# Kernel optimization log

Measured on AMD Instinct MI355X. Metric: run time of the kernel, lower is better.

The kernel has to match this reference:

```python
import jax, jax.numpy as jnp
import numpy as np
import math

V, L, D, S, F, H, B = 32000, 6, 1024, 2048, 4096, 16, 2
DK = D // H
EPS = 1e-5


def _pos_encoding(max_len, d_model):
    pos = np.arange(max_len)[:, None].astype(np.float32)
    freq = np.exp(np.arange(0, d_model, 2).astype(np.float32) * -(math.log(10000.0) / d_model))
    pe = np.zeros((max_len, d_model), dtype=np.float32)
    pe[:, 0::2] = np.sin(pos * freq)
    pe[:, 1::2] = np.cos(pos * freq)
    return jnp.asarray(pe)


def setup_inputs() -> dict:
    key = jax.random.key(0)
    ks = jax.random.split(key, 16)
    n = lambda k, shape: (jax.random.normal(k, shape, dtype=jnp.float32) * 0.02)
    return {
        "tokens": jax.random.randint(ks[0], (B, S), 0, V, dtype=jnp.int32),
        "emb": n(ks[1], (V, D)),
        "Wq": n(ks[2], (L, D, D)), "bq": jnp.zeros((L, D)),
        "Wk": n(ks[3], (L, D, D)), "bk": jnp.zeros((L, D)),
        "Wv": n(ks[4], (L, D, D)), "bv": jnp.zeros((L, D)),
        "Wo": n(ks[5], (L, D, D)), "bo": jnp.zeros((L, D)),
        "W1": n(ks[6], (L, D, F)), "b1": jnp.zeros((L, F)),
        "W2": n(ks[7], (L, F, D)), "b2": jnp.zeros((L, D)),
        "g1": jnp.ones((L, D)), "be1": jnp.zeros((L, D)),
        "g2": jnp.ones((L, D)), "be2": jnp.zeros((L, D)),
    }


def _layernorm(x, g, b):
    mu = jnp.mean(x, axis=-1, keepdims=True)
    var = jnp.var(x, axis=-1, keepdims=True)
    return (x - mu) * jax.lax.rsqrt(var + EPS) * g + b


def _encoder(tokens, emb, Wq, bq, Wk, bk, Wv, bv, Wo, bo, W1, b1, W2, b2, g1, be1, g2, be2):
    pe = _pos_encoding(S, D)
    x = emb[tokens] * jnp.float32(math.sqrt(D)) + pe  # [B,S,D]

    def layer(x, p):
        wq, bq_, wk, bk_, wv, bv_, wo, bo_, w1, b1_, w2, b2_, g1_, be1_, g2_, be2_ = p
        q = (x @ wq + bq_).reshape(B, S, H, DK)
        k = (x @ wk + bk_).reshape(B, S, H, DK)
        v = (x @ wv + bv_).reshape(B, S, H, DK)
        scores = jnp.einsum("bqhd,bkhd->bhqk", q, k) / jnp.float32(math.sqrt(DK))
        attn = jax.nn.softmax(scores, axis=-1)
        out = jnp.einsum("bhqk,bkhd->bqhd", attn, v).reshape(B, S, D)
        out = out @ wo + bo_
        x = _layernorm(x + out, g1_, be1_)
        ff = jax.nn.relu(x @ w1 + b1_) @ w2 + b2_
        x = _layernorm(x + ff, g2_, be2_)
        return x, None

    params = (Wq, bq, Wk, bk, Wv, bv, Wo, bo, W1, b1, W2, b2, g1, be1, g2, be2)
    x, _ = jax.lax.scan(layer, x, params)
    return x


def reference(tokens, emb, Wq, bq, Wk, bk, Wv, bv, Wo, bo, W1, b1, W2, b2, g1, be1, g2, be2):
    return _encoder(tokens, emb, Wq, bq, Wk, bk, Wv, bv, Wo, bo, W1, b1, W2, b2, g1, be1, g2, be2)
```

## Files before the change

kernel.cpp:

```cpp
#include <hip/hip_runtime.h>
#include <hip/hip_bf16.h>

#define DEV static __device__ __forceinline__

typedef __attribute__((ext_vector_type(8))) short bf16x8;
typedef __attribute__((ext_vector_type(4))) float f32x4;
typedef __attribute__((ext_vector_type(4))) unsigned short u16x4;
typedef __attribute__((ext_vector_type(4))) unsigned int u32x4;

constexpr int Lc = 6, Dc = 1024, Sc = 2048, Fc = 4096, Hc = 16, Bc = 2;
constexpr int Mc = Bc * Sc;
constexpr int QKVN = 3 * Dc;
constexpr float QSCALE = 0.18033688011112042f;

DEV float bf2f(unsigned short u) {
  unsigned int x = ((unsigned int)u) << 16; float f;
  __builtin_memcpy(&f, &x, 4); return f;
}
DEV unsigned short f2bf(float f) {
  unsigned int x; __builtin_memcpy(&x, &f, 4);
  x += 0x7fffu + ((x >> 16) & 1u);
  return (unsigned short)(x >> 16);
}
DEV unsigned int cvt_pk_bf16(float lo, float hi) {
  unsigned int r;
  asm("v_cvt_pk_bf16_f32 %0, %1, %2" : "=v"(r) : "v"(lo), "v"(hi));
  return r;
}

typedef __attribute__((address_space(1))) unsigned int* gas_t;
typedef __attribute__((address_space(3))) unsigned int* las_t;
DEV void gload16(const void* g, void* l) {
  __builtin_amdgcn_global_load_lds((gas_t)g, (las_t)l, 16, 0, 0);
}

DEV int vperm(int k) {
  return ((k >> 5) << 5) + (((k >> 2) & 3) << 3) + (((k >> 4) & 1) << 2) + (k & 3);
}

DEV void tr64(const float* __restrict__ W, unsigned short* __restrict__ Wt,
              int Kd, int Nd, float scale, int bx, int by, int tid,
              float (*tile)[33])
{
  const int n0 = bx * 32;
  const int tx = tid & 31, krow = tid >> 5;
  const int w = tid >> 6, lane = tid & 63;
#pragma unroll
  for (int s = 0; s < 4; ++s) {
    const int k0 = by * 256 + s * 64;
#pragma unroll
    for (int j = 0; j < 8; ++j) {
      int k = krow + j * 8;
      tile[k][tx] = W[(size_t)(k0 + k) * Nd + n0 + tx];
    }
    __syncthreads();
#pragma unroll
    for (int j = 0; j < 8; ++j) {
      int n = w * 8 + j;
      Wt[(size_t)(n0 + n) * Kd + k0 + lane] = f2bf(tile[lane][n] * scale);
    }
    __syncthreads();
  }
}

__global__ __launch_bounds__(256) void prep_weights(
    const float* __restrict__ Wq, const float* __restrict__ Wk,
    const float* __restrict__ Wv, const float* __restrict__ Wo,
    const float* __restrict__ W1, const float* __restrict__ W2,
    const float* __restrict__ bq, const float* __restrict__ bk,
    const float* __restrict__ bv,
    unsigned short* __restrict__ Wqkvt, unsigned short* __restrict__ Wot,
    unsigned short* __restrict__ W1t, unsigned short* __restrict__ W2t,
    float* __restrict__ bqkv)
{
  __shared__ float tile[64][33];
  const int l = blockIdx.x / 1548;
  const int id = blockIdx.x % 1548;
  const int t = threadIdx.x;
  const size_t owD = (size_t)l * Dc * Dc, owF = (size_t)l * Dc * Fc;
  unsigned short* Wqkvt_l = Wqkvt + (size_t)l * 3 * Dc * Dc;
  unsigned short* Wot_l = Wot + (size_t)l * Dc * Dc;
  unsigned short* W1t_l = W1t + owF;
  unsigned short* W2t_l = W2t + owF;
  if (id < 512) {
    int which = id >> 7, lo = id & 127;
    int bx = lo & 31, by = lo >> 5;
    if (which == 0)      tr64(Wq + owD, Wqkvt_l, Dc, Dc, QSCALE, bx, by, t, tile);
    else if (which == 1) tr64(Wk + owD, Wqkvt_l + (size_t)Dc * Dc, Dc, Dc, 1.0f, bx, by, t, tile);
    else if (which == 2) tr64(Wv + owD, Wqkvt_l + (size_t)2 * Dc * Dc, Dc, Dc, 1.0f, bx, by, t, tile);
    else                 tr64(Wo + owD, Wot_l, Dc, Dc, 1.0f, bx, by, t, tile);
  } else if (id < 1024) {
    int lo = id - 512;
    tr64(W1 + owF, W1t_l, Dc, Fc, 1.0f, lo & 127, lo >> 7, t, tile);
  } else if (id < 1536) {
    int lo = id - 1024;
    tr64(W2 + owF, W2t_l, Fc, Dc, 1.0f, lo & 31, lo >> 5, t, tile);
  } else {
    int i = (id - 1536) * 256 + t;
    const int ob = l * Dc;
    bqkv[l * QKVN + i] =
        (i < Dc) ? bq[ob + i] * QSCALE
                 : (i < 2 * Dc ? bk[ob + i - Dc] : bv[ob + i - 2 * Dc]);
  }
}

__global__ __launch_bounds__(256) void embed_kernel(
    const int* __restrict__ tokens, const float* __restrict__ emb,
    float* __restrict__ xf, unsigned short* __restrict__ xb)
{
  const int bs = blockIdx.x;
  const int s = bs & (Sc - 1);
  const int tok = tokens[bs];
  const int d0 = threadIdx.x * 4;
  f32x4 e4 = *(const f32x4*)(emb + (size_t)tok * Dc + d0);
  f32x4 vf; u16x4 vb;
#pragma unroll
  for (int j = 0; j < 4; ++j) {
    int d = d0 + j;
    float e = e4[j] * 32.0f;
    float fr = expf((float)(d & ~1) * (-9.210340371976184f / 1024.0f));
    float arg = (float)s * fr;
    float pe = (d & 1) ? cosf(arg) : sinf(arg);
    float v = e + pe;
    vf[j] = v; vb[j] = f2bf(v);
  }
  *(f32x4*)(xf + (size_t)bs * Dc + d0) = vf;
  *(u16x4*)(xb + (size_t)bs * Dc + d0) = vb;
}

DEV void gemm256_core(const unsigned short* __restrict__ A,
                      const unsigned short* __restrict__ Bt,
                      unsigned short (*As)[256 * 64], unsigned short (*Bs)[256 * 64],
                      f32x4 (*acc)[4], int mTile, int nTile,
                      int Kstride, int k0, int nT, int t)
{
  const int lane = t & 63;
  const int g = lane >> 4, li = lane & 15;
  const int w = t >> 6;
  const int wm = w >> 2, wn = w & 3;
  const int trow = t >> 3, tslot = t & 7;
  const int asl = tslot ^ (trow & 7);
  int aoff[4];
#pragma unroll
  for (int q = 0; q < 4; ++q) {
    int R = (trow < 32) ? (q * 32 + trow) : (96 + q * 32 + trow);
    aoff[q] = (mTile + R) * Kstride + k0 + asl * 8;
  }
  int boff[4], bld[4];
#pragma unroll
  for (int k2 = 0; k2 < 4; ++k2) {
    int idx = k2 * 512 + t;
    int br = idx >> 3;
    int bs = (idx & 7) ^ (br & 7);
    boff[k2] = (nTile + br) * Kstride + k0 + bs * 8;
    bld[k2] = idx * 8;
  }

  auto stB = [&](int nb, int kt, int ph) {
    gload16(Bt + boff[ph * 2 + 0] + kt, &Bs[nb][bld[ph * 2 + 0]]);
    gload16(Bt + boff[ph * 2 + 1] + kt, &Bs[nb][bld[ph * 2 + 1]]);
  };
  auto stA = [&](int nb, int kt, int ph) {
    gload16(A + aoff[ph * 2 + 0] + kt, &As[nb][(ph * 2 + 0) * 4096 + t * 8]);
    gload16(A + aoff[ph * 2 + 1] + kt, &As[nb][(ph * 2 + 1) * 4096 + t * 8]);
  };

  stB(0, 0, 0); stB(0, 0, 1); stA(0, 0, 0); stA(0, 0, 1);
  asm volatile("s_waitcnt vmcnt(0)" ::: "memory");
  __builtin_amdgcn_s_barrier();

  int cur = 0;
  for (int tt = 0; tt < nT; ++tt) {
    const char* Ac = (const char*)As[cur];
    const char* Bc = (const char*)Bs[cur];
    const int nb = cur ^ 1;
    const int ktn = (tt + 1) << 6;
    const bool more = tt + 1 < nT;

    bf16x8 bfr[4][2];
#pragma unroll
    for (int ni = 0; ni < 4; ++ni) {
      const int rn = wn * 64 + ni * 16 + li;
#pragma unroll
      for (int ks = 0; ks < 2; ++ks) {
        const int kb = ks * 64 + (g << 4);
        bfr[ni][ks] = *(const bf16x8*)(Bc + rn * 128 + (kb ^ ((rn & 7) << 4)));
      }
    }

#pragma unroll
    for (int ph = 0; ph < 4; ++ph) {
      bf16x8 afr[2][2];
#pragma unroll
      for (int mi2 = 0; mi2 < 2; ++mi2) {
        const int rr = wm * 32 + mi2 * 16 + li;
#pragma unroll
        for (int ks = 0; ks < 2; ++ks) {
          const int kb = ks * 64 + (g << 4);
          afr[mi2][ks] = *(const bf16x8*)(Ac + ph * 8192 + rr * 128 + (kb ^ ((rr & 7) << 4)));
        }
      }
      if (more) {
        if (ph == 0)      stB(nb, ktn, 0);
        else if (ph == 1) stB(nb, ktn, 1);
        else if (ph == 2) stA(nb, ktn, 0);
        else              stA(nb, ktn, 1);
      }
      __builtin_amdgcn_s_barrier();
      __builtin_amdgcn_s_setprio(1);
#pragma unroll
      for (int mi2 = 0; mi2 < 2; ++mi2)
#pragma unroll
        for (int ni = 0; ni < 4; ++ni)
#pragma unroll
          for (int ks = 0; ks < 2; ++ks)
            acc[ph * 2 + mi2][ni] = __builtin_amdgcn_mfma_f32_16x16x32_bf16(
                afr[mi2][ks], bfr[ni][ks], acc[ph * 2 + mi2][ni], 0, 0, 0);
      __builtin_amdgcn_s_setprio(0);
      if (ph == 0)      asm volatile("s_waitcnt vmcnt(4)" ::: "memory");
      else if (ph == 1) asm volatile("s_waitcnt vmcnt(5)" ::: "memory");
      else if (ph == 2) asm volatile("s_waitcnt vmcnt(6)" ::: "memory");
      else              asm volatile("s_waitcnt vmcnt(3)" ::: "memory");
      __builtin_amdgcn_s_barrier();
    }
    cur ^= 1;
  }
}

__global__ __launch_bounds__(512) void gemm256(
    const unsigned short* __restrict__ A, const unsigned short* __restrict__ Bt,
    const float* __restrict__ bias, unsigned short* __restrict__ outB,
    unsigned short* __restrict__ Vt, int gx, int Ndim, int Kdim, int relu)
{
  __shared__ alignas(16) unsigned short As[2][256 * 64];
  __shared__ alignas(16) unsigned short Bs[2][256 * 64];
  const int t = threadIdx.x;
  const int lane = t & 63, w = t >> 6;
  const int wm = w >> 2, wn = w & 3;
  const int g = lane >> 4, li = lane & 15;
  const int nwg = gridDim.x, flat = blockIdx.x;
  const int swz = (flat & 7) * (nwg >> 3) + (flat >> 3);
  const int mTile = (swz / gx) * 256;
  const int nTile = (swz % gx) * 256;

  f32x4 acc[8][4] = {};
  gemm256_core(A, Bt, As, Bs, acc, mTile, nTile, Kdim, 0, Kdim >> 6, t);

  const bool vblk = (Vt != nullptr) && (nTile >= 2 * Dc);
#pragma unroll
  for (int mi = 0; mi < 8; ++mi) {
#pragma unroll
    for (int ni = 0; ni < 4; ++ni) {
      const int c = nTile + wn * 64 + ni * 16 + li;
      const float bvv = bias[c];
      if (!vblk) {
#pragma unroll
        for (int j = 0; j < 4; ++j) {
          const int r = mTile + wm * 128 + mi * 16 + g * 4 + j;
          float v = acc[mi][ni][j] + bvv;
          if (relu) v = fmaxf(v, 0.0f);
          outB[(size_t)r * Ndim + c] = f2bf(v);
        }
      } else {
        const int r0 = mTile + wm * 128 + mi * 16 + g * 4;
        const int b = r0 >> 11, s0 = r0 & 2047;
        const int sp = (s0 & ~63) + vperm(s0 & 63);
        u16x4 ov;
#pragma unroll
        for (int j = 0; j < 4; ++j) ov[j] = f2bf(acc[mi][ni][j] + bvv);
        *(u16x4*)(Vt + ((size_t)(b * Dc + (c - 2 * Dc))) * Sc + sp) = ov;
      }
    }
  }
}

template<int SPLIT>
__global__ __launch_bounds__(512) void gemm256_sk(
    const unsigned short* __restrict__ A, const unsigned short* __restrict__ Bt,
    unsigned short* __restrict__ part, int gx, int gy, int Ndim, int Ktot)
{
  __shared__ alignas(16) unsigned short As[2][256 * 64];
  __shared__ alignas(16) unsigned short Bs[2][256 * 64];
  const int t = threadIdx.x;
  const int lane = t & 63, w = t >> 6;
  const int wm = w >> 2, wn = w & 3;
  const int g = lane >> 4, li = lane & 15;
  const int nwg = gridDim.x, flat = blockIdx.x;
  const int swz = (flat & 7) * (nwg >> 3) + (flat >> 3);
  const int nTile = (swz % gx) * 256;
  const int mTile = ((swz / gx) % gy) * 256;
  const int z = swz / (gx * gy);
  const int Kseg = Ktot / SPLIT;

  f32x4 acc[8][4] = {};
  gemm256_core(A, Bt, As, Bs, acc, mTile, nTile, Ktot, z * Kseg, Kseg >> 6, t);

  unsigned short* po = part + (size_t)z * Mc * Ndim;
#pragma unroll
  for (int mi = 0; mi < 8; ++mi)
#pragma unroll
    for (int ni = 0; ni < 4; ++ni) {
      const int c = nTile + wn * 64 + ni * 16 + li;
#pragma unroll
      for (int j = 0; j < 4; ++j) {
        const int r = mTile + wm * 128 + mi * 16 + g * 4 + j;
        po[(size_t)r * Ndim + c] = f2bf(acc[mi][ni][j]);
      }
    }
}

__global__ __launch_bounds__(256) void attn128(
    const unsigned short* __restrict__ QKV, const unsigned short* __restrict__ Vt,
    unsigned short* __restrict__ O)
{
  __shared__ alignas(16) unsigned short Qs[128 * 64];
  __shared__ alignas(16) unsigned short Ks[2][64 * 64];
  __shared__ alignas(16) unsigned short Vs[2][64 * 64];

  const int t = threadIdx.x;
  const int lane = t & 63, w = t >> 6;
  const int g = lane >> 4, li = lane & 15;
  const int flat = blockIdx.x;
  const int idx = ((flat & 7) << 6) | (flat >> 3);
  const int qb = idx & 15, bh = idx >> 4;
  const int b = bh >> 4, h = bh & 15;

  const size_t qbase  = ((size_t)(b * Sc + qb * 128)) * QKVN + h * 64;
  const size_t kbase0 = ((size_t)b * Sc) * QKVN + Dc + h * 64;
  const size_t vbase0 = ((size_t)(b * Dc + h * 64)) * Sc;

#pragma unroll
  for (int i = 0; i < 4; ++i) {
    int idx2 = i * 256 + t, row = idx2 >> 3, sl = (idx2 & 7) ^ (row & 7);
    gload16(QKV + qbase + (size_t)row * QKVN + sl * 8, &Qs[idx2 * 8]);
  }
  const unsigned short* kg[2];
  const unsigned short* vg[2];
  int loff[2];
#pragma unroll
  for (int i = 0; i < 2; ++i) {
    int idx2 = i * 256 + t, row = idx2 >> 3, sl = (idx2 & 7) ^ (row & 7);
    kg[i] = QKV + kbase0 + (size_t)row * QKVN + sl * 8;
    vg[i] = Vt + vbase0 + (size_t)row * Sc + sl * 8;
    loff[i] = idx2 * 8;
  }
  gload16(kg[0], &Ks[0][loff[0]]); gload16(kg[1], &Ks[0][loff[1]]);
  gload16(vg[0], &Vs[0][loff[0]]); gload16(vg[1], &Vs[0][loff[1]]);
  kg[0] += 64 * QKVN; kg[1] += 64 * QKVN;
  vg[0] += 64;        vg[1] += 64;
  __syncthreads();

  bf16x8 qf[2][2];
#pragma unroll
  for (int qi = 0; qi < 2; ++qi) {
    const int rq = w * 32 + qi * 16 + li;
#pragma unroll
    for (int ks = 0; ks < 2; ++ks) {
      const int kb = ks * 64 + (g << 4);
      qf[qi][ks] = *(const bf16x8*)((const char*)Qs + rq * 128 + (kb ^ ((rq & 7) << 4)));
    }
  }
  bf16x8 ones;
#pragma unroll
  for (int e = 0; e < 8; ++e) ones[e] = (short)0x3F80;

  f32x4 acc_o[2][4] = {};
  f32x4 acc_l[2] = {};
  int cur = 0;

  for (int kc = 0; kc < Sc; kc += 64) {
    if (kc + 64 < Sc) {
      const int nxt = cur ^ 1;
      gload16(kg[0], &Ks[nxt][loff[0]]); gload16(kg[1], &Ks[nxt][loff[1]]);
      gload16(vg[0], &Vs[nxt][loff[0]]); gload16(vg[1], &Vs[nxt][loff[1]]);
      kg[0] += 64 * QKVN; kg[1] += 64 * QKVN;
      vg[0] += 64;        vg[1] += 64;
    }

    f32x4 accs[2][4] = {};
#pragma unroll
    for (int ks = 0; ks < 2; ++ks) {
      const int kb = ks * 64 + (g << 4);
#pragma unroll
      for (int ni = 0; ni < 4; ++ni) {
        int rk = ni * 16 + li;
        bf16x8 ak = *(const bf16x8*)((const char*)Ks[cur] + rk * 128 + (kb ^ ((rk & 7) << 4)));
        accs[0][ni] = __builtin_amdgcn_mfma_f32_16x16x32_bf16(ak, qf[0][ks], accs[0][ni], 0, 0, 0);
        accs[1][ni] = __builtin_amdgcn_mfma_f32_16x16x32_bf16(ak, qf[1][ks], accs[1][ni], 0, 0, 0);
      }
    }

    unsigned int pk[2][4][2];
#pragma unroll
    for (int qi = 0; qi < 2; ++qi)
#pragma unroll
      for (int ni = 0; ni < 4; ++ni) {
        float p0 = exp2f(accs[qi][ni][0]);
        float p1 = exp2f(accs[qi][ni][1]);
        float p2 = exp2f(accs[qi][ni][2]);
        float p3 = exp2f(accs[qi][ni][3]);
        pk[qi][ni][0] = cvt_pk_bf16(p0, p1);
        pk[qi][ni][1] = cvt_pk_bf16(p2, p3);
      }

#pragma unroll
    for (int ks = 0; ks < 2; ++ks) {
      bf16x8 ap[2];
#pragma unroll
      for (int qi = 0; qi < 2; ++qi) {
        u32x4 av = {pk[qi][2 * ks][0], pk[qi][2 * ks][1],
                    pk[qi][2 * ks + 1][0], pk[qi][2 * ks + 1][1]};
        ap[qi] = __builtin_bit_cast(bf16x8, av);
        acc_l[qi] = __builtin_amdgcn_mfma_f32_16x16x32_bf16(ap[qi], ones, acc_l[qi], 0, 0, 0);
      }
      const int kb = ks * 64 + (g << 4);
#pragma unroll
      for (int ni = 0; ni < 4; ++ni) {
        int rd = ni * 16 + li;
        bf16x8 bv = *(const bf16x8*)((const char*)Vs[cur] + rd * 128 + (kb ^ ((rd & 7) << 4)));
        acc_o[0][ni] = __builtin_amdgcn_mfma_f32_16x16x32_bf16(ap[0], bv, acc_o[0][ni], 0, 0, 0);
        acc_o[1][ni] = __builtin_amdgcn_mfma_f32_16x16x32_bf16(ap[1], bv, acc_o[1][ni], 0, 0, 0);
      }
    }

    __syncthreads();
    cur ^= 1;
  }

  const size_t obase = ((size_t)(b * Sc + qb * 128)) * Dc + h * 64;
#pragma unroll
  for (int qi = 0; qi < 2; ++qi) {
    float denom[4];
#pragma unroll
    for (int j = 0; j < 4; ++j) denom[j] = 1.0f / acc_l[qi][j];
#pragma unroll
    for (int ni = 0; ni < 4; ++ni)
#pragma unroll
      for (int j = 0; j < 4; ++j) {
        int q = w * 32 + qi * 16 + g * 4 + j;
        O[obase + (size_t)q * Dc + ni * 16 + li] = f2bf(acc_o[qi][ni][j] * denom[j]);
      }
  }
}

template<int SPLIT>
__global__ __launch_bounds__(256) void reduce_ln(
    const unsigned short* __restrict__ part, const float* __restrict__ bias,
    const float* __restrict__ res, const float* __restrict__ g,
    const float* __restrict__ be, float* __restrict__ xf_out,
    unsigned short* __restrict__ xb_out)
{
  const int row = blockIdx.x, t = threadIdx.x;
  const size_t off = (size_t)row * Dc + t * 4;
  f32x4 v = *(const f32x4*)(res + off);
  v += *(const f32x4*)(bias + t * 4);
#pragma unroll
  for (int s = 0; s < SPLIT; ++s) {
    u16x4 pv = *(const u16x4*)(part + (size_t)s * Mc * Dc + off);
#pragma unroll
    for (int j = 0; j < 4; ++j) v[j] += bf2f(pv[j]);
  }

  float sm = v[0] + v[1] + v[2] + v[3];
  float q = v[0]*v[0] + v[1]*v[1] + v[2]*v[2] + v[3]*v[3];
#pragma unroll
  for (int o = 32; o; o >>= 1) {
    sm += __shfl_down(sm, o);
    q += __shfl_down(q, o);
  }
  __shared__ float rs_[4], rq_[4];
  const int lane = t & 63, w = t >> 6;
  if (lane == 0) { rs_[w] = sm; rq_[w] = q; }
  __syncthreads();
  sm = rs_[0] + rs_[1] + rs_[2] + rs_[3];
  q = rq_[0] + rq_[1] + rq_[2] + rq_[3];
  const float mu = sm * (1.0f / 1024.0f);
  const float var = q * (1.0f / 1024.0f) - mu * mu;
  const float rstd = rsqrtf(var + 1e-5f);
  f32x4 vg = *(const f32x4*)(g + t * 4);
  f32x4 vb = *(const f32x4*)(be + t * 4);
  f32x4 o; u16x4 ob;
#pragma unroll
  for (int j = 0; j < 4; ++j) {
    float val = (v[j] - mu) * rstd * vg[j] + vb[j];
    o[j] = val; ob[j] = f2bf(val);
  }
  *(f32x4*)(xf_out + off) = o;
  *(u16x4*)(xb_out + off) = ob;
}

extern "C" void kernel_launch(void* const* d_in, const int* in_sizes, int n_in,
                              void* d_out, int out_size, void* d_ws, size_t ws_size,
                              hipStream_t stream)
{
  (void)in_sizes; (void)n_in; (void)out_size; (void)ws_size;
  const int*   tokens = (const int*)d_in[0];
  const float* emb = (const float*)d_in[1];
  const float* Wq = (const float*)d_in[2];
  const float* bq = (const float*)d_in[3];
  const float* Wk = (const float*)d_in[4];
  const float* bk = (const float*)d_in[5];
  const float* Wv = (const float*)d_in[6];
  const float* bv = (const float*)d_in[7];
  const float* Wo = (const float*)d_in[8];
  const float* bo = (const float*)d_in[9];
  const float* W1 = (const float*)d_in[10];
  const float* b1 = (const float*)d_in[11];
  const float* W2 = (const float*)d_in[12];
  const float* b2 = (const float*)d_in[13];
  const float* g1 = (const float*)d_in[14];
  const float* be1 = (const float*)d_in[15];
  const float* g2 = (const float*)d_in[16];
  const float* be2 = (const float*)d_in[17];

  char* p = (char*)d_ws;
  auto take = [&](size_t bytes) { char* q = p; p += bytes; return q; };
  unsigned short* Wqkvt = (unsigned short*)take((size_t)Lc * 3 * Dc * Dc * 2);
  unsigned short* Wot = (unsigned short*)take((size_t)Lc * Dc * Dc * 2);
  unsigned short* W1t = (unsigned short*)take((size_t)Lc * Dc * Fc * 2);
  unsigned short* W2t = (unsigned short*)take((size_t)Lc * Fc * Dc * 2);
  float*          bqkv = (float*)take((size_t)Lc * QKVN * 4);
  float*          xf  = (float*)take((size_t)Mc * Dc * 4);
  unsigned short* xb  = (unsigned short*)take((size_t)Mc * Dc * 2);
  unsigned short* QKVb = (unsigned short*)take((size_t)Mc * QKVN * 2);
  unsigned short* Vtb = (unsigned short*)take((size_t)Bc * Dc * Sc * 2);
  unsigned short* Ob  = (unsigned short*)take((size_t)Mc * Dc * 2);
  unsigned short* ff1 = (unsigned short*)take((size_t)Mc * Fc * 2);
  unsigned short* part = QKVb;

  dim3 blk(256);
  prep_weights<<<dim3(Lc * 1548), blk, 0, stream>>>(
      Wq, Wk, Wv, Wo, W1, W2, bq, bk, bv, Wqkvt, Wot, W1t, W2t, bqkv);
  embed_kernel<<<dim3(Mc), blk, 0, stream>>>(tokens, emb, xf, xb);

  for (int l = 0; l < Lc; ++l) {
    const int ob = l * Dc;
    const unsigned short* Wqkvt_l = Wqkvt + (size_t)l * 3 * Dc * Dc;
    const unsigned short* Wot_l = Wot + (size_t)l * Dc * Dc;
    const unsigned short* W1t_l = W1t + (size_t)l * Dc * Fc;
    const unsigned short* W2t_l = W2t + (size_t)l * Fc * Dc;

    gemm256<<<dim3((Mc / 256) * (QKVN / 256)), dim3(512), 0, stream>>>(
        xb, Wqkvt_l, bqkv + l * QKVN, QKVb, Vtb, QKVN / 256, QKVN, Dc, 0);
    attn128<<<dim3(512), blk, 0, stream>>>(QKVb, Vtb, Ob);

    gemm256_sk<4><<<dim3((Dc / 256) * (Mc / 256) * 4), dim3(512), 0, stream>>>(
        Ob, Wot_l, part, Dc / 256, Mc / 256, Dc, Dc);
    reduce_ln<4><<<dim3(Mc), blk, 0, stream>>>(
        part, bo + ob, xf, g1 + ob, be1 + ob, xf, xb);

    gemm256<<<dim3((Mc / 256) * (Fc / 256)), dim3(512), 0, stream>>>(
        xb, W1t_l, b1 + l * Fc, ff1, nullptr, Fc / 256, Fc, Dc, 1);

    gemm256_sk<4><<<dim3((Dc / 256) * (Mc / 256) * 4), dim3(512), 0, stream>>>(
        ff1, W2t_l, part, Dc / 256, Mc / 256, Dc, Fc);
    reduce_ln<4><<<dim3(Mc), blk, 0, stream>>>(
        part, b2 + ob, xf, g2 + ob, be2 + ob,
        (l == Lc - 1) ? (float*)d_out : xf, xb);
  }
}
```

Measured before the change: 1.420 ms.

## Vectorize weight transpose tiles and drop fp32 residual stream for bf16

The weight-prep transpose now works on 64x64 tiles with 16-byte float4 loads and 8-byte packed bf16 stores, halving the block count. The fp32 residual buffer is also removed: the embedding writes only bf16, and each LayerNorm reads its residual from the bf16 activation and writes fp32 only for the final output. This cuts global memory traffic in prep_weights, embed and reduce_ln. In exchange the residual path is held only in bf16, which adds rounding error that accumulates across the layers.

```diff
diff --git a/kernel.cpp b/kernel.cpp
--- a/kernel.cpp
+++ b/kernel.cpp
@@ -38,26 +38,29 @@
   return ((k >> 5) << 5) + (((k >> 2) & 3) << 3) + (((k >> 4) & 1) << 2) + (k & 3);
 }
 
-DEV void tr64(const float* __restrict__ W, unsigned short* __restrict__ Wt,
-              int Kd, int Nd, float scale, int bx, int by, int tid,
-              float (*tile)[33])
-{
-  const int n0 = bx * 32;
-  const int tx = tid & 31, krow = tid >> 5;
-  const int w = tid >> 6, lane = tid & 63;
+DEV void tr64v(const float* __restrict__ W, unsigned short* __restrict__ Wt,
+               int Kd, int Nd, float scale, int bx, int by, int tid,
+               float (*tile)[65])
+{
+  const int n0 = bx * 64;
 #pragma unroll
   for (int s = 0; s < 4; ++s) {
     const int k0 = by * 256 + s * 64;
 #pragma unroll
-    for (int j = 0; j < 8; ++j) {
-      int k = krow + j * 8;
-      tile[k][tx] = W[(size_t)(k0 + k) * Nd + n0 + tx];
+    for (int it = 0; it < 4; ++it) {
+      int idx = it * 256 + tid;
+      int k = idx >> 4, c0 = (idx & 15) * 4;
+      *(f32x4*)&tile[k][c0] = *(const f32x4*)&W[(size_t)(k0 + k) * Nd + n0 + c0];
     }
     __syncthreads();
 #pragma unroll
-    for (int j = 0; j < 8; ++j) {
-      int n = w * 8 + j;
-      Wt[(size_t)(n0 + n) * Kd + k0 + lane] = f2bf(tile[lane][n] * scale);
+    for (int it = 0; it < 4; ++it) {
+      int idx = it * 256 + tid;
+      int n = idx >> 4, kc = (idx & 15) * 4;
+      u16x4 o;
+#pragma unroll
+      for (int j = 0; j < 4; ++j) o[j] = f2bf(tile[kc + j][n] * scale);
+      *(u16x4*)&Wt[(size_t)(n0 + n) * Kd + k0 + kc] = o;
     }
     __syncthreads();
   }
@@ -73,30 +76,30 @@
     unsigned short* __restrict__ W1t, unsigned short* __restrict__ W2t,
     float* __restrict__ bqkv)
 {
-  __shared__ float tile[64][33];
-  const int l = blockIdx.x / 1548;
-  const int id = blockIdx.x % 1548;
+  __shared__ float tile[64][65];
+  const int l = blockIdx.x / 780;
+  const int id = blockIdx.x % 780;
   const int t = threadIdx.x;
   const size_t owD = (size_t)l * Dc * Dc, owF = (size_t)l * Dc * Fc;
   unsigned short* Wqkvt_l = Wqkvt + (size_t)l * 3 * Dc * Dc;
   unsigned short* Wot_l = Wot + (size_t)l * Dc * Dc;
   unsigned short* W1t_l = W1t + owF;
   unsigned short* W2t_l = W2t + owF;
-  if (id < 512) {
-    int which = id >> 7, lo = id & 127;
-    int bx = lo & 31, by = lo >> 5;
-    if (which == 0)      tr64(Wq + owD, Wqkvt_l, Dc, Dc, QSCALE, bx, by, t, tile);
-    else if (which == 1) tr64(Wk + owD, Wqkvt_l + (size_t)Dc * Dc, Dc, Dc, 1.0f, bx, by, t, tile);
-    else if (which == 2) tr64(Wv + owD, Wqkvt_l + (size_t)2 * Dc * Dc, Dc, Dc, 1.0f, bx, by, t, tile);
-    else                 tr64(Wo + owD, Wot_l, Dc, Dc, 1.0f, bx, by, t, tile);
-  } else if (id < 1024) {
+  if (id < 256) {
+    int which = id >> 6, lo = id & 63;
+    int bx = lo & 15, by = lo >> 4;
+    if (which == 0)      tr64v(Wq + owD, Wqkvt_l, Dc, Dc, QSCALE, bx, by, t, tile);
+    else if (which == 1) tr64v(Wk + owD, Wqkvt_l + (size_t)Dc * Dc, Dc, Dc, 1.0f, bx, by, t, tile);
+    else if (which == 2) tr64v(Wv + owD, Wqkvt_l + (size_t)2 * Dc * Dc, Dc, Dc, 1.0f, bx, by, t, tile);
+    else                 tr64v(Wo + owD, Wot_l, Dc, Dc, 1.0f, bx, by, t, tile);
+  } else if (id < 512) {
+    int lo = id - 256;
+    tr64v(W1 + owF, W1t_l, Dc, Fc, 1.0f, lo & 63, lo >> 6, t, tile);
+  } else if (id < 768) {
     int lo = id - 512;
-    tr64(W1 + owF, W1t_l, Dc, Fc, 1.0f, lo & 127, lo >> 7, t, tile);
-  } else if (id < 1536) {
-    int lo = id - 1024;
-    tr64(W2 + owF, W2t_l, Fc, Dc, 1.0f, lo & 31, lo >> 5, t, tile);
+    tr64v(W2 + owF, W2t_l, Fc, Dc, 1.0f, lo & 15, lo >> 4, t, tile);
   } else {
-    int i = (id - 1536) * 256 + t;
+    int i = (id - 768) * 256 + t;
     const int ob = l * Dc;
     bqkv[l * QKVN + i] =
         (i < Dc) ? bq[ob + i] * QSCALE
@@ -106,14 +109,14 @@
 
 __global__ __launch_bounds__(256) void embed_kernel(
     const int* __restrict__ tokens, const float* __restrict__ emb,
-    float* __restrict__ xf, unsigned short* __restrict__ xb)
+    unsigned short* __restrict__ xb)
 {
   const int bs = blockIdx.x;
   const int s = bs & (Sc - 1);
   const int tok = tokens[bs];
   const int d0 = threadIdx.x * 4;
   f32x4 e4 = *(const f32x4*)(emb + (size_t)tok * Dc + d0);
-  f32x4 vf; u16x4 vb;
+  u16x4 vb;
 #pragma unroll
   for (int j = 0; j < 4; ++j) {
     int d = d0 + j;
@@ -121,10 +124,8 @@
     float fr = expf((float)(d & ~1) * (-9.210340371976184f / 1024.0f));
     float arg = (float)s * fr;
     float pe = (d & 1) ? cosf(arg) : sinf(arg);
-    float v = e + pe;
-    vf[j] = v; vb[j] = f2bf(v);
-  }
-  *(f32x4*)(xf + (size_t)bs * Dc + d0) = vf;
+    vb[j] = f2bf(e + pe);
+  }
   *(u16x4*)(xb + (size_t)bs * Dc + d0) = vb;
 }
 
@@ -446,13 +447,16 @@
 template<int SPLIT>
 __global__ __launch_bounds__(256) void reduce_ln(
     const unsigned short* __restrict__ part, const float* __restrict__ bias,
-    const float* __restrict__ res, const float* __restrict__ g,
-    const float* __restrict__ be, float* __restrict__ xf_out,
+    const unsigned short* __restrict__ resb, const float* __restrict__ g,
+    const float* __restrict__ be, float* __restrict__ fout,
     unsigned short* __restrict__ xb_out)
 {
   const int row = blockIdx.x, t = threadIdx.x;
   const size_t off = (size_t)row * Dc + t * 4;
-  f32x4 v = *(const f32x4*)(res + off);
+  u16x4 rv = *(const u16x4*)(resb + off);
+  f32x4 v;
+#pragma unroll
+  for (int j = 0; j < 4; ++j) v[j] = bf2f(rv[j]);
   v += *(const f32x4*)(bias + t * 4);
 #pragma unroll
   for (int s = 0; s < SPLIT; ++s) {
@@ -485,7 +489,7 @@
     float val = (v[j] - mu) * rstd * vg[j] + vb[j];
     o[j] = val; ob[j] = f2bf(val);
   }
-  *(f32x4*)(xf_out + off) = o;
+  if (fout) *(f32x4*)(fout + off) = o;
   *(u16x4*)(xb_out + off) = ob;
 }
 
@@ -520,7 +524,6 @@
   unsigned short* W1t = (unsigned short*)take((size_t)Lc * Dc * Fc * 2);
   unsigned short* W2t = (unsigned short*)take((size_t)Lc * Fc * Dc * 2);
   float*          bqkv = (float*)take((size_t)Lc * QKVN * 4);
-  float*          xf  = (float*)take((size_t)Mc * Dc * 4);
   unsigned short* xb  = (unsigned short*)take((size_t)Mc * Dc * 2);
   unsigned short* QKVb = (unsigned short*)take((size_t)Mc * QKVN * 2);
   unsigned short* Vtb = (unsigned short*)take((size_t)Bc * Dc * Sc * 2);
@@ -529,9 +532,9 @@
   unsigned short* part = QKVb;
 
   dim3 blk(256);
-  prep_weights<<<dim3(Lc * 1548), blk, 0, stream>>>(
+  prep_weights<<<dim3(Lc * 780), blk, 0, stream>>>(
       Wq, Wk, Wv, Wo, W1, W2, bq, bk, bv, Wqkvt, Wot, W1t, W2t, bqkv);
-  embed_kernel<<<dim3(Mc), blk, 0, stream>>>(tokens, emb, xf, xb);
+  embed_kernel<<<dim3(Mc), blk, 0, stream>>>(tokens, emb, xb);
 
   for (int l = 0; l < Lc; ++l) {
     const int ob = l * Dc;
@@ -547,7 +550,7 @@
     gemm256_sk<4><<<dim3((Dc / 256) * (Mc / 256) * 4), dim3(512), 0, stream>>>(
         Ob, Wot_l, part, Dc / 256, Mc / 256, Dc, Dc);
     reduce_ln<4><<<dim3(Mc), blk, 0, stream>>>(
-        part, bo + ob, xf, g1 + ob, be1 + ob, xf, xb);
+        part, bo + ob, xb, g1 + ob, be1 + ob, nullptr, xb);
 
     gemm256<<<dim3((Mc / 256) * (Fc / 256)), dim3(512), 0, stream>>>(
         xb, W1t_l, b1 + l * Fc, ff1, nullptr, Fc / 256, Fc, Dc, 1);
@@ -555,7 +558,7 @@
     gemm256_sk<4><<<dim3((Dc / 256) * (Mc / 256) * 4), dim3(512), 0, stream>>>(
         ff1, W2t_l, part, Dc / 256, Mc / 256, Dc, Fc);
     reduce_ln<4><<<dim3(Mc), blk, 0, stream>>>(
-        part, b2 + ob, xf, g2 + ob, be2 + ob,
-        (l == Lc - 1) ? (float*)d_out : xf, xb);
-  }
-}
+        part, b2 + ob, xb, g2 + ob, be2 + ob,
+        (l == Lc - 1) ? (float*)d_out : nullptr, xb);
+  }
+}
```

After: 1.382 ms. 1.03x faster.
